# Kernel tuning notes

Hardware: AMD Instinct MI355X
Metric: run time of the kernel (lower is better)

Reference implementation:

```python
import jax, jax.numpy as jnp
import numpy as np

EPSILON = 0.05
SINKHORN_ITERS = 3
TEMP = 0.1
PROB_RATIO = 1.0
LAMBD = 15.0
MU = 1.0
NU = 1.0
GAMMA = 0.2

B, D, K = 16384, 512, 2048


def setup_inputs() -> dict:
    key = jax.random.key(0)
    k1, k2, k3 = jax.random.split(key, 3)
    z_1 = jax.random.normal(k1, (B, D), dtype=jnp.float32)
    z_2 = jax.random.normal(k2, (B, D), dtype=jnp.float32)
    W = jax.random.normal(k3, (K, D), dtype=jnp.float32) * (1.0 / np.sqrt(D))
    return {"z_1": z_1, "z_2": z_2, "W": W}


def _compute_v(z):
    # unbiased variance over batch dim, matching torch.var default
    var = jnp.var(z, axis=0, ddof=1)
    return jnp.mean(jnp.maximum(0.0, GAMMA - jnp.sqrt(var + 1e-8)))


def _compute_c(z):
    n, d = z.shape
    zc = z - jnp.mean(z, axis=0, keepdims=True)
    C = (zc.T @ zc) / (n - 1)  # [d, d] unbiased covariance (torch.cov)
    off = C - jnp.diag(jnp.diag(C))
    return jnp.sum(off * off) / d


def _l2norm(z):
    return z / jnp.clip(jnp.linalg.norm(z, axis=-1, keepdims=True), 1e-12)


def _sinkhorn(out):
    # out: [B, K] raw logits (no grad path)
    b, k = out.shape
    Q = jnp.exp(out / EPSILON).T  # [K, B]
    Q = Q / jnp.sum(Q)
    for _ in range(SINKHORN_ITERS):
        Q = Q / (jnp.sum(Q, axis=1, keepdims=True) * k)
        Q = Q / (jnp.sum(Q, axis=0, keepdims=True) * b)
    Q = Q * b
    return Q.T  # [B, K]


def reference(z_1, z_2, W):
    v_z1 = _compute_v(z_1)
    v_z2 = _compute_v(z_2)
    c_z1 = _compute_c(z_1)
    c_z2 = _compute_c(z_2)

    z1n = _l2norm(z_1)
    z2n = _l2norm(z_2)
    logits_1 = z1n @ W.T  # [B, K]
    logits_2 = z2n @ W.T

    tgt_w_1 = jax.lax.stop_gradient(logits_1 * PROB_RATIO + logits_2 * (1 - PROB_RATIO))
    tgt_w_2 = jax.lax.stop_gradient(logits_2 * PROB_RATIO + logits_1 * (1 - PROB_RATIO))
    tgt_probs_1 = _sinkhorn(tgt_w_1)
    tgt_probs_2 = _sinkhorn(tgt_w_2)

    l1 = logits_1 / TEMP
    l2 = logits_2 / TEMP
    lp1 = jax.nn.log_softmax(l1, axis=1)
    lp2 = jax.nn.log_softmax(l2, axis=1)

    loss_ce = -0.5 * (jnp.mean(jnp.sum(tgt_probs_1 * lp2, axis=1))
                      + jnp.mean(jnp.sum(tgt_probs_2 * lp1, axis=1)))
    loss_var = v_z1 + v_z2
    loss_cov = c_z1 + c_z2
    loss = LAMBD * loss_ce + MU * loss_var + NU * loss_cov

    # diagnostics (no-grad in original)
    logits = jnp.concatenate([l1, l2], axis=0)  # [2B, K]
    k_idx = jnp.argmax(logits, axis=-1)
    hard_probs = jnp.zeros((K,), logits.dtype).at[k_idx].add(1.0) / logits.shape[0]
    code_perplexity = jnp.exp(-jnp.sum(hard_probs * jnp.log(hard_probs + 1e-7)))
    avg_probs = jnp.mean(jax.nn.softmax(logits, axis=-1), axis=0)
    prob_perplexity = jnp.exp(-jnp.sum(avg_probs * jnp.log(avg_probs + 1e-7)))
    acc_1 = jnp.mean((jnp.argmax(l1, axis=1) == jnp.argmax(tgt_probs_2, axis=1)).astype(jnp.float32))
    acc_2 = jnp.mean((jnp.argmax(l2, axis=1) == jnp.argmax(tgt_probs_1, axis=1)).astype(jnp.float32))
    acc = 0.5 * (acc_1 + acc_2)

    return (loss, loss_ce, loss_var, loss_cov, code_perplexity, prob_perplexity, acc)
```

## Files before the change

kernel.cpp:

```cpp
#include <hip/hip_runtime.h>
#include <hip/hip_bf16.h>

#define B_N 16384
#define D_N 512
#define K_N 2048

typedef __attribute__((ext_vector_type(8))) short bf16x8;
typedef __attribute__((ext_vector_type(4))) float f32x4;
typedef __attribute__((ext_vector_type(4))) unsigned short u16x4;
typedef unsigned short u16;

__device__ __forceinline__ float bf2f(short s) {
  return __builtin_bit_cast(float, ((unsigned)(u16)s) << 16);
}
__device__ __forceinline__ u16 f2bf(float x) {
  return __builtin_bit_cast(u16, __float2bfloat16(x));
}
__device__ __forceinline__ unsigned fbits(float x) {
  return __builtin_bit_cast(unsigned, x);
}
__device__ __forceinline__ float wred_sum(float v) {
#pragma unroll
  for (int o = 32; o; o >>= 1) v += __shfl_down(v, o, 64);
  return v;
}

__device__ __forceinline__ void gld16(const u16* g, const u16* l) {
  __builtin_amdgcn_global_load_lds((const __attribute__((address_space(1))) void*)g,
                                   (__attribute__((address_space(3))) void*)l, 16, 0, 0);
}

__global__ __launch_bounds__(256) void k_rownorm(const float* __restrict__ z1,
                                                 const float* __restrict__ z2,
                                                 u16* __restrict__ zn1, u16* __restrict__ zn2,
                                                 u16* __restrict__ zb1, u16* __restrict__ zb2) {
  int wid = threadIdx.x >> 6, lane = threadIdx.x & 63;
  int row = blockIdx.x * 4 + wid;
  const float* z; u16 *zn, *zb; int r;
  if (row < B_N) { z = z1; zn = zn1; zb = zb1; r = row; }
  else { z = z2; zn = zn2; zb = zb2; r = row - B_N; }
  const float4* zr = (const float4*)(z + (size_t)r * D_N);
  float4 va = zr[lane], vb = zr[lane + 64];
  float ss = va.x*va.x + va.y*va.y + va.z*va.z + va.w*va.w
           + vb.x*vb.x + vb.y*vb.y + vb.z*vb.z + vb.w*vb.w;
#pragma unroll
  for (int o = 32; o; o >>= 1) ss += __shfl_xor(ss, o, 64);
  float inv = 1.0f / fmaxf(sqrtf(ss), 1e-12f);
  u16x4 pa = {f2bf(va.x), f2bf(va.y), f2bf(va.z), f2bf(va.w)};
  u16x4 pb = {f2bf(vb.x), f2bf(vb.y), f2bf(vb.z), f2bf(vb.w)};
  u16x4 na = {f2bf(va.x*inv), f2bf(va.y*inv), f2bf(va.z*inv), f2bf(va.w*inv)};
  u16x4 nb = {f2bf(vb.x*inv), f2bf(vb.y*inv), f2bf(vb.z*inv), f2bf(vb.w*inv)};
  ((u16x4*)(zb + (size_t)r * D_N))[lane] = pa;
  ((u16x4*)(zb + (size_t)r * D_N))[lane + 64] = pb;
  ((u16x4*)(zn + (size_t)r * D_N))[lane] = na;
  ((u16x4*)(zn + (size_t)r * D_N))[lane + 64] = nb;
}

__global__ __launch_bounds__(256) void k_convW(const float* __restrict__ W,
                                               u16* __restrict__ Wb) {
  size_t base = ((size_t)blockIdx.x * 256 + threadIdx.x) * 8;
#pragma unroll
  for (int j = 0; j < 8; j++) Wb[base + j] = f2bf(W[base + j]);
}

__global__ __launch_bounds__(512) void k_colstats(const u16* __restrict__ zb1,
                                                  const u16* __restrict__ zb2,
                                                  float* __restrict__ csum,
                                                  float* __restrict__ csumsq) {
  int zi = blockIdx.z;
  const u16* z = zi ? zb2 : zb1;
  __shared__ float s1[512], s2[512];
  int t = threadIdx.y * 64 + threadIdx.x;
  s1[t] = 0.f; s2[t] = 0.f;
  __syncthreads();
  int c0 = threadIdx.x * 8;
  float a[8], a2[8];
#pragma unroll
  for (int e = 0; e < 8; e++) { a[e] = 0.f; a2[e] = 0.f; }
  for (int u = 0; u < 16; u++) {
    int r = blockIdx.y * 128 + threadIdx.y + 8 * u;
    bf16x8 v = *(const bf16x8*)&z[(size_t)r * D_N + c0];
#pragma unroll
    for (int e = 0; e < 8; e++) { float x = bf2f(v[e]); a[e] += x; a2[e] += x * x; }
  }
#pragma unroll
  for (int e = 0; e < 8; e++) {
    atomicAdd(&s1[c0 + e], a[e]);
    atomicAdd(&s2[c0 + e], a2[e]);
  }
  __syncthreads();
  atomicAdd(&csum[zi * D_N + t], s1[t]);
  atomicAdd(&csumsq[zi * D_N + t], s2[t]);
}

__global__ __launch_bounds__(256) void k_vloss(const float* __restrict__ csum,
                                               const float* __restrict__ csumsq,
                                               float* __restrict__ scal) {
  int idx = blockIdx.x * 256 + threadIdx.x;
  float s = csum[idx], sq = csumsq[idx];
  float mean = s * (1.0f / (float)B_N);
  float var = (sq - (float)B_N * mean * mean) * (1.0f / (float)(B_N - 1));
  float term = fmaxf(0.f, 0.2f - sqrtf(var + 1e-8f));
  term = wred_sum(term);
  __shared__ float sw[4];
  if ((threadIdx.x & 63) == 0) sw[threadIdx.x >> 6] = term;
  __syncthreads();
  if (threadIdx.x == 0) atomicAdd(&scal[0], sw[0] + sw[1] + sw[2] + sw[3]);
}

__global__ __launch_bounds__(256) void k_gram(const u16* __restrict__ zb1,
                                              const u16* __restrict__ zb2,
                                              float* __restrict__ Gpart) {
  int zi = blockIdx.z >> 4, chunk = blockIdx.z & 15;
  const u16* z = zi ? zb2 : zb1;
  int ti = 0, xx = blockIdx.x;
  while (xx >= 8 - ti) { xx -= 8 - ti; ti++; }
  int tj = ti + xx;
  int i0 = ti * 64, j0 = tj * 64;
  __shared__ u16 lA[64][32], lB[64][32];
  int t = threadIdx.x, wid = t >> 6, lane = t & 63;
  int br = t & 31, fg = t >> 5;
  f32x4 acc[4];
#pragma unroll
  for (int q = 0; q < 4; q++) acc[q] = (f32x4){0.f, 0.f, 0.f, 0.f};
  for (int bb = 0; bb < 1024; bb += 32) {
    size_t rb = ((size_t)chunk * 1024 + bb + br) * D_N;
    bf16x8 va = *(const bf16x8*)&z[rb + i0 + fg * 8];
    bf16x8 vb = *(const bf16x8*)&z[rb + j0 + fg * 8];
#pragma unroll
    for (int e = 0; e < 8; e++) {
      lA[fg * 8 + e][br] = (u16)va[e];
      lB[fg * 8 + e][br] = (u16)vb[e];
    }
    __syncthreads();
    int m = lane & 15, q = lane >> 4;
    bf16x8 a = *(const bf16x8*)&lA[16 * wid + m][8 * q];
#pragma unroll
    for (int tt = 0; tt < 4; tt++) {
      bf16x8 b = *(const bf16x8*)&lB[16 * tt + m][8 * q];
      acc[tt] = __builtin_amdgcn_mfma_f32_16x16x32_bf16(a, b, acc[tt], 0, 0, 0);
    }
    __syncthreads();
  }
  float* gp = Gpart + (((size_t)zi * 16 + chunk) * 36 + blockIdx.x) * 4096;
  int n = lane & 15, q = lane >> 4;
#pragma unroll
  for (int tt = 0; tt < 4; tt++)
#pragma unroll
    for (int r = 0; r < 4; r++)
      gp[(16 * wid + q * 4 + r) * 64 + 16 * tt + n] = acc[tt][r];
}

__global__ __launch_bounds__(256) void k_covreduce(const float* __restrict__ Gpart,
                                                   const float* __restrict__ csum,
                                                   float* __restrict__ scal) {
  int zi = blockIdx.y;
  int tile = blockIdx.x >> 4, part = blockIdx.x & 15;
  int ti = 0, xx = tile;
  while (xx >= 8 - ti) { xx -= 8 - ti; ti++; }
  int tj = ti + xx;
  int idx = part * 256 + threadIdx.x;
  int li = idx >> 6, lj = idx & 63;
  int i = ti * 64 + li, j = tj * 64 + lj;
  float g = 0.f;
#pragma unroll
  for (int c = 0; c < 16; c++)
    g += Gpart[(((size_t)zi * 16 + c) * 36 + tile) * 4096 + idx];
  float mi = csum[zi * D_N + i] * (1.0f / (float)B_N);
  float mj = csum[zi * D_N + j] * (1.0f / (float)B_N);
  float C = (g - (float)B_N * mi * mj) * (1.0f / (float)(B_N - 1));
  float wgt = (ti == tj) ? ((li == lj) ? 0.f : 1.f) : 2.f;
  float v = wgt * C * C;
  v = wred_sum(v);
  __shared__ float sw[4];
  if ((threadIdx.x & 63) == 0) sw[threadIdx.x >> 6] = v;
  __syncthreads();
  if (threadIdx.x == 0) atomicAdd(&scal[1], sw[0] + sw[1] + sw[2] + sw[3]);
}

__global__ __launch_bounds__(256) void k_logits(const u16* __restrict__ zn1,
                                                const u16* __restrict__ zn2,
                                                const u16* __restrict__ Wb,
                                                u16* __restrict__ L1, u16* __restrict__ L2,
                                                float* __restrict__ rowsum) {
  int zi = blockIdx.z;
  const u16* A = zi ? zn2 : zn1;
  u16* Lout = zi ? L2 : L1;
  int b0 = blockIdx.x * 128, k0 = blockIdx.y * 128;
  __shared__ u16 lA[128 * 32], lB[128 * 32];
  int t = threadIdx.x, lane = t & 63, wid = t >> 6;
  int wm = wid >> 1, wn = wid & 1;
  f32x4 acc[4][4];
#pragma unroll
  for (int i = 0; i < 4; i++)
#pragma unroll
    for (int j = 0; j < 4; j++) acc[i][j] = (f32x4){0.f, 0.f, 0.f, 0.f};
  int row0 = t >> 2, seg0 = (t & 3) * 8;
  int ldsoff = (t & 192) * 16;
  for (int d0 = 0; d0 < D_N; d0 += 32) {
    gld16(A + (size_t)(b0 + row0) * D_N + d0 + seg0, (const u16*)((const char*)lA + ldsoff));
    gld16(A + (size_t)(b0 + 64 + row0) * D_N + d0 + seg0, (const u16*)((const char*)lA + 4096 + ldsoff));
    gld16(Wb + (size_t)(k0 + row0) * D_N + d0 + seg0, (const u16*)((const char*)lB + ldsoff));
    gld16(Wb + (size_t)(k0 + 64 + row0) * D_N + d0 + seg0, (const u16*)((const char*)lB + 4096 + ldsoff));
    __syncthreads();
    bf16x8 af[4], bfr[4];
#pragma unroll
    for (int i = 0; i < 4; i++)
      af[i] = *(const bf16x8*)&lA[(wm * 64 + i * 16 + (lane & 15)) * 32 + (lane >> 4) * 8];
#pragma unroll
    for (int j = 0; j < 4; j++)
      bfr[j] = *(const bf16x8*)&lB[(wn * 64 + j * 16 + (lane & 15)) * 32 + (lane >> 4) * 8];
#pragma unroll
    for (int i = 0; i < 4; i++)
#pragma unroll
      for (int j = 0; j < 4; j++)
        acc[i][j] = __builtin_amdgcn_mfma_f32_16x16x32_bf16(af[i], bfr[j], acc[i][j], 0, 0, 0);
    __syncthreads();
  }
  int cq = lane >> 4, cn = lane & 15;
  float rpart[4] = {0.f, 0.f, 0.f, 0.f};
#pragma unroll
  for (int i = 0; i < 4; i++)
#pragma unroll
    for (int j = 0; j < 4; j++)
#pragma unroll
      for (int r = 0; r < 4; r++) {
        u16 h = f2bf(acc[i][j][r]);
        int gb = b0 + wm * 64 + i * 16 + cq * 4 + r;
        int gk = k0 + wn * 64 + j * 16 + cn;
        Lout[(size_t)gb * K_N + gk] = h;
        rpart[j] += __expf(20.0f * bf2f((short)h));
      }
  float* red = (float*)lA;
  if (t < 128) red[t] = 0.f;
  __syncthreads();
#pragma unroll
  for (int j = 0; j < 4; j++) atomicAdd(&red[wn * 64 + j * 16 + cn], rpart[j]);
  __syncthreads();
  if (t < 128) atomicAdd(&rowsum[(size_t)zi * 3 * K_N + k0 + t], red[t]);
}

__global__ __launch_bounds__(256) void k_sink(const u16* __restrict__ L1,
                                              const u16* __restrict__ L2,
                                              float* __restrict__ rowsum, int it) {
  int zi = blockIdx.y;
  const u16* L = zi ? L2 : L1;
  const float* rs_in = rowsum + ((size_t)zi * 3 + it) * K_N;
  float* rs_out = rowsum + ((size_t)zi * 3 + it + 1) * K_N;
  __shared__ float pm[K_N];
  int t = threadIdx.x, lane = t & 63, wid = t >> 6;
  for (int k = t; k < K_N; k += 256) pm[k] = 0.f;
  float rv[32];
#pragma unroll
  for (int jj = 0; jj < 4; jj++) {
    const float4* p = (const float4*)&rs_in[jj * 512 + lane * 8];
    float4 x = p[0], y = p[1];
    rv[jj*8+0] = 1.0f / ((float)K_N * x.x); rv[jj*8+1] = 1.0f / ((float)K_N * x.y);
    rv[jj*8+2] = 1.0f / ((float)K_N * x.z); rv[jj*8+3] = 1.0f / ((float)K_N * x.w);
    rv[jj*8+4] = 1.0f / ((float)K_N * y.x); rv[jj*8+5] = 1.0f / ((float)K_N * y.y);
    rv[jj*8+6] = 1.0f / ((float)K_N * y.z); rv[jj*8+7] = 1.0f / ((float)K_N * y.w);
  }
  __syncthreads();
  float racc[32];
#pragma unroll
  for (int q = 0; q < 32; q++) racc[q] = 0.f;
  int w = blockIdx.x * 4 + wid;
  for (int rr = 0; rr < 8; rr++) {
    int b = w * 8 + rr;
    float ex[32];
    float c = 0.f;
#pragma unroll
    for (int jj = 0; jj < 4; jj++) {
      bf16x8 v = *(const bf16x8*)&L[(size_t)b * K_N + jj * 512 + lane * 8];
#pragma unroll
      for (int e = 0; e < 8; e++) {
        float E = __expf(20.0f * bf2f(v[e]));
        ex[jj * 8 + e] = E;
        c += E * rv[jj * 8 + e];
      }
    }
#pragma unroll
    for (int o = 32; o; o >>= 1) c += __shfl_xor(c, o, 64);
    float cb = 1.0f / ((float)B_N * c);
#pragma unroll
    for (int q = 0; q < 32; q++) racc[q] += ex[q] * cb;
  }
#pragma unroll
  for (int q = 0; q < 32; q++)
    atomicAdd(&pm[(q & 7) * 256 + (q >> 3) * 64 + lane], racc[q]);
  __syncthreads();
  for (int k = t; k < K_N; k += 256)
    atomicAdd(&rs_out[k], pm[(k & 7) * 256 + (k >> 3)]);
}

__global__ __launch_bounds__(256, 2) void k_final(const u16* __restrict__ L1,
                                                  const u16* __restrict__ L2,
                                                  const float* __restrict__ rowsum,
                                                  float* __restrict__ probsum,
                                                  int* __restrict__ counts,
                                                  float* __restrict__ scal) {
  __shared__ float pmerge[K_N];
  const float* rs1 = rowsum + 2 * K_N;
  const float* rs2 = rowsum + 5 * K_N;
  int t = threadIdx.x, lane = t & 63, wid = t >> 6;
  for (int k = t; k < K_N; k += 256) pmerge[k] = 0.f;
  float rv1[32], rv2[32];
#pragma unroll
  for (int jj = 0; jj < 4; jj++) {
    const float4* p1 = (const float4*)&rs1[jj * 512 + lane * 8];
    const float4* p2 = (const float4*)&rs2[jj * 512 + lane * 8];
    float4 x1 = p1[0], y1 = p1[1], x2 = p2[0], y2 = p2[1];
    rv1[jj*8+0] = 1.0f/((float)K_N*x1.x); rv1[jj*8+1] = 1.0f/((float)K_N*x1.y);
    rv1[jj*8+2] = 1.0f/((float)K_N*x1.z); rv1[jj*8+3] = 1.0f/((float)K_N*x1.w);
    rv1[jj*8+4] = 1.0f/((float)K_N*y1.x); rv1[jj*8+5] = 1.0f/((float)K_N*y1.y);
    rv1[jj*8+6] = 1.0f/((float)K_N*y1.z); rv1[jj*8+7] = 1.0f/((float)K_N*y1.w);
    rv2[jj*8+0] = 1.0f/((float)K_N*x2.x); rv2[jj*8+1] = 1.0f/((float)K_N*x2.y);
    rv2[jj*8+2] = 1.0f/((float)K_N*x2.z); rv2[jj*8+3] = 1.0f/((float)K_N*x2.w);
    rv2[jj*8+4] = 1.0f/((float)K_N*y2.x); rv2[jj*8+5] = 1.0f/((float)K_N*y2.y);
    rv2[jj*8+6] = 1.0f/((float)K_N*y2.z); rv2[jj*8+7] = 1.0f/((float)K_N*y2.w);
  }
  __syncthreads();
  float pacc[32];
#pragma unroll
  for (int q = 0; q < 32; q++) pacc[q] = 0.f;
  float ce_acc = 0.f; int acc_cnt = 0;
  int w = blockIdx.x * 4 + wid;
  for (int pp = 0; pp < 8; pp++) {
    int ba = w * 16 + pp * 2;
    bf16x8 va1[4], va2[4], vb1[4], vb2[4];
#pragma unroll
    for (int jj = 0; jj < 4; jj++) {
      va1[jj] = *(const bf16x8*)&L1[(size_t)ba * K_N + jj * 512 + lane * 8];
      va2[jj] = *(const bf16x8*)&L2[(size_t)ba * K_N + jj * 512 + lane * 8];
      vb1[jj] = *(const bf16x8*)&L1[(size_t)(ba + 1) * K_N + jj * 512 + lane * 8];
      vb2[jj] = *(const bf16x8*)&L2[(size_t)(ba + 1) * K_N + jj * 512 + lane * 8];
    }
    float sE1a=0,sE2a=0,d12a=0,d21a=0,Z1a=0,Z2a=0;
    float sE1b=0,sE2b=0,d12b=0,d21b=0,Z1b=0,Z2b=0;
    unsigned um1a=0,um2a=0,ua1a=0,ua2a=0;
    unsigned um1b=0,um2b=0,ua1b=0,ua2b=0;
#pragma unroll
    for (int jj = 0; jj < 4; jj++)
#pragma unroll
      for (int e = 0; e < 8; e++) {
        int q = jj * 8 + e;
        unsigned ik = 2047u - (unsigned)(jj * 512 + lane * 8 + e);
        float x1 = bf2f(va1[jj][e]), x2 = bf2f(va2[jj][e]);
        float t1 = __expf(10.0f * x1), t2 = __expf(10.0f * x2);
        float e1 = t1 * t1 * rv1[q], e2 = t2 * t2 * rv2[q];
        sE1a += e1; sE2a += e2; d12a += e1 * x2; d21a += e2 * x1; Z1a += t1; Z2a += t2;
        um1a = max(um1a, (fbits(t1) & 0xFFFFF800u) | ik);
        um2a = max(um2a, (fbits(t2) & 0xFFFFF800u) | ik);
        ua1a = max(ua1a, (fbits(e1) & 0xFFFFF800u) | ik);
        ua2a = max(ua2a, (fbits(e2) & 0xFFFFF800u) | ik);
        x1 = bf2f(vb1[jj][e]); x2 = bf2f(vb2[jj][e]);
        t1 = __expf(10.0f * x1); t2 = __expf(10.0f * x2);
        e1 = t1 * t1 * rv1[q]; e2 = t2 * t2 * rv2[q];
        sE1b += e1; sE2b += e2; d12b += e1 * x2; d21b += e2 * x1; Z1b += t1; Z2b += t2;
        um1b = max(um1b, (fbits(t1) & 0xFFFFF800u) | ik);
        um2b = max(um2b, (fbits(t2) & 0xFFFFF800u) | ik);
        ua1b = max(ua1b, (fbits(e1) & 0xFFFFF800u) | ik);
        ua2b = max(ua2b, (fbits(e2) & 0xFFFFF800u) | ik);
      }
#pragma unroll
    for (int o = 32; o; o >>= 1) {
      sE1a += __shfl_xor(sE1a, o, 64); sE2a += __shfl_xor(sE2a, o, 64);
      d12a += __shfl_xor(d12a, o, 64); d21a += __shfl_xor(d21a, o, 64);
      Z1a += __shfl_xor(Z1a, o, 64);   Z2a += __shfl_xor(Z2a, o, 64);
      sE1b += __shfl_xor(sE1b, o, 64); sE2b += __shfl_xor(sE2b, o, 64);
      d12b += __shfl_xor(d12b, o, 64); d21b += __shfl_xor(d21b, o, 64);
      Z1b += __shfl_xor(Z1b, o, 64);   Z2b += __shfl_xor(Z2b, o, 64);
      um1a = max(um1a, (unsigned)__shfl_xor((int)um1a, o, 64));
      um2a = max(um2a, (unsigned)__shfl_xor((int)um2a, o, 64));
      ua1a = max(ua1a, (unsigned)__shfl_xor((int)ua1a, o, 64));
      ua2a = max(ua2a, (unsigned)__shfl_xor((int)ua2a, o, 64));
      um1b = max(um1b, (unsigned)__shfl_xor((int)um1b, o, 64));
      um2b = max(um2b, (unsigned)__shfl_xor((int)um2b, o, 64));
      ua1b = max(ua1b, (unsigned)__shfl_xor((int)ua1b, o, 64));
      ua2b = max(ua2b, (unsigned)__shfl_xor((int)ua2b, o, 64));
    }
    {
      int m1i = 2047 - (int)(um1a & 2047u), m2i = 2047 - (int)(um2a & 2047u);
      int a1i = 2047 - (int)(ua1a & 2047u), a2i = 2047 - (int)(ua2a & 2047u);
      float invc1 = 1.0f / sE1a, invc2 = 1.0f / sE2a;
      ce_acc += (10.0f * d12a) * invc1 - __logf(Z2a) + (10.0f * d21a) * invc2 - __logf(Z1a);
      acc_cnt += (m1i == a2i) + (m2i == a1i);
      if (lane == 0) { atomicAdd(&counts[m1i], 1); atomicAdd(&counts[m2i], 1); }
      float iZ1 = 1.0f / Z1a, iZ2 = 1.0f / Z2a;
#pragma unroll
      for (int jj = 0; jj < 4; jj++)
#pragma unroll
        for (int e = 0; e < 8; e++)
          pacc[jj * 8 + e] += __expf(10.0f * bf2f(va1[jj][e])) * iZ1
                            + __expf(10.0f * bf2f(va2[jj][e])) * iZ2;
    }
    {
      int m1i = 2047 - (int)(um1b & 2047u), m2i = 2047 - (int)(um2b & 2047u);
      int a1i = 2047 - (int)(ua1b & 2047u), a2i = 2047 - (int)(ua2b & 2047u);
      float invc1 = 1.0f / sE1b, invc2 = 1.0f / sE2b;
      ce_acc += (10.0f * d12b) * invc1 - __logf(Z2b) + (10.0f * d21b) * invc2 - __logf(Z1b);
      acc_cnt += (m1i == a2i) + (m2i == a1i);
      if (lane == 0) { atomicAdd(&counts[m1i], 1); atomicAdd(&counts[m2i], 1); }
      float iZ1 = 1.0f / Z1b, iZ2 = 1.0f / Z2b;
#pragma unroll
      for (int jj = 0; jj < 4; jj++)
#pragma unroll
        for (int e = 0; e < 8; e++)
          pacc[jj * 8 + e] += __expf(10.0f * bf2f(vb1[jj][e])) * iZ1
                            + __expf(10.0f * bf2f(vb2[jj][e])) * iZ2;
    }
  }
  if (lane == 0) {
    atomicAdd(&scal[2], ce_acc);
    atomicAdd(&scal[3], (float)acc_cnt);
  }
#pragma unroll
  for (int q = 0; q < 32; q++)
    atomicAdd(&pmerge[(q & 7) * 256 + (q >> 3) * 64 + lane], pacc[q]);
  __syncthreads();
  for (int k = t; k < K_N; k += 256) atomicAdd(&probsum[k], pmerge[k]);
}

__global__ __launch_bounds__(256) void k_combine(const float* __restrict__ scal,
                                                 const float* __restrict__ probsum,
                                                 const int* __restrict__ counts,
                                                 float* __restrict__ out) {
  int t = threadIdx.x;
  float ec = 0.f, ep = 0.f;
  for (int k = t; k < K_N; k += 256) {
    float p = (float)counts[k] * (1.0f / (2.0f * (float)B_N));
    ec += -p * __logf(p + 1e-7f);
    float q = probsum[k] * (1.0f / (2.0f * (float)B_N));
    ep += -q * __logf(q + 1e-7f);
  }
  ec = wred_sum(ec);
  ep = wred_sum(ep);
  __shared__ float se[4], sp[4];
  if ((t & 63) == 0) { se[t >> 6] = ec; sp[t >> 6] = ep; }
  __syncthreads();
  if (t == 0) {
    float tec = se[0] + se[1] + se[2] + se[3];
    float tep = sp[0] + sp[1] + sp[2] + sp[3];
    float ce = -0.5f * scal[2] * (1.0f / (float)B_N);
    float lvar = scal[0] * (1.0f / (float)D_N);
    float lcov = scal[1] * (1.0f / (float)D_N);
    float acc = scal[3] * (1.0f / (2.0f * (float)B_N));
    out[0] = 15.0f * ce + lvar + lcov;
    out[1] = ce;
    out[2] = lvar;
    out[3] = lcov;
    out[4] = __expf(tec);
    out[5] = __expf(tep);
    out[6] = acc;
  }
}

extern "C" void kernel_launch(void* const* d_in, const int* in_sizes, int n_in,
                              void* d_out, int out_size, void* d_ws, size_t ws_size,
                              hipStream_t stream) {
  (void)in_sizes; (void)n_in; (void)out_size; (void)ws_size;
  const float* z1 = (const float*)d_in[0];
  const float* z2 = (const float*)d_in[1];
  const float* W = (const float*)d_in[2];

  char* w = (char*)d_ws;
  size_t off = 0;
  auto take = [&](size_t b) -> void* {
    void* p = w + off;
    off = (off + b + 255) & ~(size_t)255;
    return p;
  };
  float* rowsum = (float*)take(2 * 3 * K_N * 4);
  float* csum = (float*)take(2 * D_N * 4);
  float* csumsq = (float*)take(2 * D_N * 4);
  float* probsum = (float*)take(K_N * 4);
  int* counts = (int*)take(K_N * 4);
  float* scal = (float*)take(64);
  size_t zero_bytes = off;
  u16* zn1 = (u16*)take((size_t)B_N * D_N * 2);
  u16* zn2 = (u16*)take((size_t)B_N * D_N * 2);
  u16* Wb = (u16*)take((size_t)K_N * D_N * 2);
  u16* L1 = (u16*)take((size_t)B_N * K_N * 2);
  u16* L2 = (u16*)take((size_t)B_N * K_N * 2);
  float* Gpart = (float*)take((size_t)2 * 16 * 36 * 4096 * 4);
  u16* zb1 = L1;
  u16* zb2 = L1 + (size_t)B_N * D_N;

  hipMemsetAsync(d_ws, 0, zero_bytes, stream);

  k_rownorm<<<8192, 256, 0, stream>>>(z1, z2, zn1, zn2, zb1, zb2);
  k_convW<<<512, 256, 0, stream>>>(W, Wb);
  k_colstats<<<dim3(1, 128, 2), dim3(64, 8), 0, stream>>>(zb1, zb2, csum, csumsq);
  k_vloss<<<4, 256, 0, stream>>>(csum, csumsq, scal);
  k_gram<<<dim3(36, 1, 32), 256, 0, stream>>>(zb1, zb2, Gpart);
  k_covreduce<<<dim3(36 * 16, 2), 256, 0, stream>>>(Gpart, csum, scal);
  k_logits<<<dim3(128, 16, 2), 256, 0, stream>>>(zn1, zn2, Wb, L1, L2, rowsum);
  k_sink<<<dim3(512, 2), 256, 0, stream>>>(L1, L2, rowsum, 0);
  k_sink<<<dim3(512, 2), 256, 0, stream>>>(L1, L2, rowsum, 1);
  k_final<<<256, 256, 0, stream>>>(L1, L2, rowsum, probsum, counts, scal);
  k_combine<<<1, 256, 0, stream>>>(scal, probsum, counts, (float*)d_out);
}
```

Baseline: 547.8 us.

## Deepen logits GEMM K-tile to 64 with swizzled LDS and vectorized stores

The logits GEMM now stages 64-wide K slices per iteration, halving the barrier count per tile. The LDS layout is XOR-swizzled to avoid bank conflicts on fragment reads. MFMA operands are swapped so each lane holds four consecutive K columns, which allows 8-byte vector stores of the bf16 logits. The per-column exp sums are reduced with cross-lane shuffles before the shared atomics, which cuts LDS atomic traffic. LDS use doubles, which may reduce occupancy.

```diff
diff --git a/kernel.cpp b/kernel.cpp
--- a/kernel.cpp
+++ b/kernel.cpp
@@ -187,7 +187,7 @@
   const u16* A = zi ? zn2 : zn1;
   u16* Lout = zi ? L2 : L1;
   int b0 = blockIdx.x * 128, k0 = blockIdx.y * 128;
-  __shared__ u16 lA[128 * 32], lB[128 * 32];
+  __shared__ u16 lA[128 * 64], lB[128 * 64];
   int t = threadIdx.x, lane = t & 63, wid = t >> 6;
   int wm = wid >> 1, wn = wid & 1;
   f32x4 acc[4][4];
@@ -195,47 +195,76 @@
   for (int i = 0; i < 4; i++)
 #pragma unroll
     for (int j = 0; j < 4; j++) acc[i][j] = (f32x4){0.f, 0.f, 0.f, 0.f};
-  int row0 = t >> 2, seg0 = (t & 3) * 8;
+  int srow = t >> 3;
+  int sseg = t & 7;
   int ldsoff = (t & 192) * 16;
-  for (int d0 = 0; d0 < D_N; d0 += 32) {
-    gld16(A + (size_t)(b0 + row0) * D_N + d0 + seg0, (const u16*)((const char*)lA + ldsoff));
-    gld16(A + (size_t)(b0 + 64 + row0) * D_N + d0 + seg0, (const u16*)((const char*)lA + 4096 + ldsoff));
-    gld16(Wb + (size_t)(k0 + row0) * D_N + d0 + seg0, (const u16*)((const char*)lB + ldsoff));
-    gld16(Wb + (size_t)(k0 + 64 + row0) * D_N + d0 + seg0, (const u16*)((const char*)lB + 4096 + ldsoff));
+  for (int d0 = 0; d0 < D_N; d0 += 64) {
+#pragma unroll
+    for (int qo = 0; qo < 4; qo++) {
+      int row = qo * 32 + srow;
+      int scol = (sseg ^ (row & 7)) * 8;
+      gld16(A + (size_t)(b0 + row) * D_N + d0 + scol,
+            (const u16*)((const char*)lA + qo * 4096 + ldsoff));
+      gld16(Wb + (size_t)(k0 + row) * D_N + d0 + scol,
+            (const u16*)((const char*)lB + qo * 4096 + ldsoff));
+    }
     __syncthreads();
-    bf16x8 af[4], bfr[4];
-#pragma unroll
-    for (int i = 0; i < 4; i++)
-      af[i] = *(const bf16x8*)&lA[(wm * 64 + i * 16 + (lane & 15)) * 32 + (lane >> 4) * 8];
-#pragma unroll
-    for (int j = 0; j < 4; j++)
-      bfr[j] = *(const bf16x8*)&lB[(wn * 64 + j * 16 + (lane & 15)) * 32 + (lane >> 4) * 8];
-#pragma unroll
-    for (int i = 0; i < 4; i++)
-#pragma unroll
-      for (int j = 0; j < 4; j++)
-        acc[i][j] = __builtin_amdgcn_mfma_f32_16x16x32_bf16(af[i], bfr[j], acc[i][j], 0, 0, 0);
+#pragma unroll
+    for (int ks = 0; ks < 2; ks++) {
+      bf16x8 af[4], bfr[4];
+#pragma unroll
+      for (int i = 0; i < 4; i++) {
+        int row = wm * 64 + i * 16 + (lane & 15);
+        int seg = (ks * 4 + (lane >> 4)) ^ (row & 7);
+        af[i] = *(const bf16x8*)((const char*)lA + row * 128 + seg * 16);
+      }
+#pragma unroll
+      for (int j = 0; j < 4; j++) {
+        int row = wn * 64 + j * 16 + (lane & 15);
+        int seg = (ks * 4 + (lane >> 4)) ^ (row & 7);
+        bfr[j] = *(const bf16x8*)((const char*)lB + row * 128 + seg * 16);
+      }
+#pragma unroll
+      for (int i = 0; i < 4; i++)
+#pragma unroll
+        for (int j = 0; j < 4; j++)
+          acc[i][j] = __builtin_amdgcn_mfma_f32_16x16x32_bf16(bfr[j], af[i], acc[i][j], 0, 0, 0);
+    }
     __syncthreads();
   }
-  int cq = lane >> 4, cn = lane & 15;
-  float rpart[4] = {0.f, 0.f, 0.f, 0.f};
-#pragma unroll
-  for (int i = 0; i < 4; i++)
-#pragma unroll
-    for (int j = 0; j < 4; j++)
-#pragma unroll
-      for (int r = 0; r < 4; r++) {
-        u16 h = f2bf(acc[i][j][r]);
-        int gb = b0 + wm * 64 + i * 16 + cq * 4 + r;
-        int gk = k0 + wn * 64 + j * 16 + cn;
-        Lout[(size_t)gb * K_N + gk] = h;
-        rpart[j] += __expf(20.0f * bf2f((short)h));
-      }
   float* red = (float*)lA;
   if (t < 128) red[t] = 0.f;
   __syncthreads();
-#pragma unroll
-  for (int j = 0; j < 4; j++) atomicAdd(&red[wn * 64 + j * 16 + cn], rpart[j]);
+  int cb = lane & 15;
+  int cq = lane >> 4;
+  float rp[16];
+#pragma unroll
+  for (int q = 0; q < 16; q++) rp[q] = 0.f;
+#pragma unroll
+  for (int i = 0; i < 4; i++)
+#pragma unroll
+    for (int j = 0; j < 4; j++) {
+      f32x4 v = acc[i][j];
+      u16x4 h = {f2bf(v[0]), f2bf(v[1]), f2bf(v[2]), f2bf(v[3])};
+      int gb = b0 + wm * 64 + i * 16 + cb;
+      int gk = k0 + wn * 64 + j * 16 + cq * 4;
+      *(u16x4*)&Lout[(size_t)gb * K_N + gk] = h;
+#pragma unroll
+      for (int r = 0; r < 4; r++)
+        rp[j * 4 + r] += __expf(20.0f * bf2f((short)h[r]));
+    }
+#pragma unroll
+  for (int q = 0; q < 16; q++) {
+#pragma unroll
+    for (int o = 1; o < 16; o <<= 1) rp[q] += __shfl_xor(rp[q], o, 64);
+  }
+  if (cb == 0) {
+#pragma unroll
+    for (int j = 0; j < 4; j++)
+#pragma unroll
+      for (int r = 0; r < 4; r++)
+        atomicAdd(&red[wn * 64 + j * 16 + cq * 4 + r], rp[j * 4 + r]);
+  }
   __syncthreads();
   if (t < 128) atomicAdd(&rowsum[(size_t)zi * 3 * K_N + k0 + t], red[t]);
 }
```

Result: no change. 552.3 us (+0.8%).
